# Performance work log

Measured on AMD Instinct MI355X. Metric: run time of the kernel, lower is better.

## Reference

```python
import jax, jax.numpy as jnp
import numpy as np

B, S, D, H = 2, 2048, 2048, 16
HD = D // H  # head_dim = 128


def setup_inputs() -> dict:
    key = jax.random.key(0)
    ks = jax.random.split(key, 7)
    s = 0.02
    return {
        "q": jax.random.normal(ks[0], (B, S, D), jnp.float32),
        "k": jax.random.normal(ks[1], (B, S, D), jnp.float32),
        "v": jax.random.normal(ks[2], (B, S, D), jnp.float32),
        "wq": jax.random.normal(ks[3], (D, D), jnp.float32) * s,
        "wk": jax.random.normal(ks[4], (D, D), jnp.float32) * s,
        "wv": jax.random.normal(ks[5], (D, D), jnp.float32) * s,
        "wo": jax.random.normal(ks[6], (D, D), jnp.float32) * s,
    }


def reference(q, k, v, wq, wk, wv, wo):
    # Linear(bias=False): y = x @ W.T  (torch weight layout [out, in])
    xq = jnp.einsum("bse,me->bsm", q, wq).reshape(B, S, H, HD).transpose(0, 2, 1, 3)
    xk = jnp.einsum("bse,me->bsm", k, wk).reshape(B, S, H, HD).transpose(0, 2, 1, 3)
    xv = jnp.einsum("bse,me->bsm", v, wv).reshape(B, S, H, HD).transpose(0, 2, 1, 3)
    scores = jnp.einsum("bhqd,bhkd->bhqk", xq, xk) / jnp.sqrt(jnp.float32(HD))
    # causal mask: -inf above diagonal
    causal = jnp.tril(jnp.ones((S, S), dtype=bool))
    scores = jnp.where(causal[None, None], scores, jnp.float32(-jnp.inf))
    probs = jax.nn.softmax(scores.astype(jnp.float32), axis=-1)
    out = jnp.einsum("bhqk,bhkd->bhqd", probs, xv)  # [B,H,S,HD]
    out = out.transpose(0, 2, 1, 3).reshape(B, S, D)
    out = jnp.einsum("bsm,em->bse", out, wo)
    return out
```

## Files before the change

### kernel.cpp

```cpp
#include <hip/hip_runtime.h>

typedef __bf16 bf16x8 __attribute__((ext_vector_type(8)));
typedef float f32x4 __attribute__((ext_vector_type(4)));

__device__ inline unsigned short f2bf(float f) {
  unsigned int u = __float_as_uint(f);
  u = (u + 0x7FFFu + ((u >> 16) & 1u)) >> 16;
  return (unsigned short)u;
}

__device__ inline void gl_lds16(const void* g, void* l) {
  __builtin_amdgcn_global_load_lds(
      (__attribute__((address_space(1))) const void*)g,
      (__attribute__((address_space(3))) void*)l, 16, 0, 0);
}

__global__ __launch_bounds__(256) void cvt_batch(const float* __restrict__ p0,
                                                 const float* __restrict__ p1,
                                                 const float* __restrict__ p2,
                                                 const float* __restrict__ p3,
                                                 unsigned short* __restrict__ out,
                                                 int n4each) {
  const int y = blockIdx.y;
  const float* src = (y == 0) ? p0 : (y == 1) ? p1 : (y == 2) ? p2 : p3;
  unsigned short* dst = out + (size_t)y * n4each * 4;
  int i = blockIdx.x * 256 + threadIdx.x;
  if (i >= n4each) return;
  const float4 v = ((const float4*)src)[i];
  ushort4 o;
  o.x = f2bf(v.x); o.y = f2bf(v.y); o.z = f2bf(v.z); o.w = f2bf(v.w);
  ((ushort4*)dst)[i] = o;
}

template <int MODE>
__global__ __launch_bounds__(512, 2) void gemm8(const unsigned short* __restrict__ A,
                                                const unsigned short* __restrict__ Wb,
                                                void* __restrict__ Cv,
                                                int N, int Kloop, int lda,
                                                float qscale) {
  extern __shared__ char lds[];
  const int tid = threadIdx.x;
  const int w = tid >> 6, l = tid & 63;
  const int wr = w >> 2, wc = w & 3;

  const int nbx = N >> 8;
  const int cpx = gridDim.x >> 3;
  const int bid = blockIdx.x;
  const int swz = (bid & 7) * cpx + (bid >> 3);
  const int by = swz / nbx, bx = swz % nbx;
  const int m0 = by << 7, n0 = bx << 8;

  const unsigned short* W = Wb;
  const unsigned short* Ab = A;
  float scale = 1.0f;
  int seg = 0;
  if (MODE == 0) {
    seg = m0 >> 12;
    W = Wb + (size_t)seg * 2048 * 2048;
    scale = (seg == 0) ? qscale : 1.0f;
  }

  const int col_l = ((l & 3) * 8) ^ ((l >= 32) ? 16 : 0);
  const size_t rowA0 = (size_t)(m0 + w * 16 + (l >> 2)) * lda + col_l;
  const size_t rowB0 = (size_t)(n0 + w * 16 + (l >> 2)) * lda + col_l;
  const size_t rowB1 = rowB0 + (size_t)128 * lda;
  const int stA = w * 2048;

  const int Sread = ((l & 15) * 64 + (l >> 4) * 16) ^ ((l & 8) << 2);
  const int ldsAr = Sread;
  const int ldsBr = 16384 + (wc >> 1) * 16384 + Sread;

  const f32x4 fz = {0.f, 0.f, 0.f, 0.f};
  f32x4 acc[4][4];
#pragma unroll
  for (int i = 0; i < 4; i++)
#pragma unroll
    for (int j = 0; j < 4; j++) acc[i][j] = fz;
  bf16x8 afA[2][2], afB[2][2], bfr[2][4];

#define STAGE_A(pb, kb)                               \
  gl_lds16(Ab + rowA0 + (kb), (pb) + stA);            \
  gl_lds16(Ab + rowA0 + (kb) + 32, (pb) + stA + 1024)

#define STAGE_B(pb, h, kb)                                                \
  gl_lds16(W + ((h) ? rowB1 : rowB0) + (kb),                              \
           (pb) + 16384 + (h) * 16384 + stA);                             \
  gl_lds16(W + ((h) ? rowB1 : rowB0) + (kb) + 32,                         \
           (pb) + 16384 + (h) * 16384 + stA + 1024)

#define LDF(dst, pb, qi)                                                       \
  _Pragma("unroll") for (int i = 0; i < 2; ++i) {                              \
    dst[0][i] =                                                                \
        *(const bf16x8*)((pb) + ldsAr + (wr * 4 + (qi) * 2 + i) * 2048);       \
    dst[1][i] = *(const bf16x8*)((pb) + ldsAr +                                \
                                 (wr * 4 + (qi) * 2 + i) * 2048 + 1024);       \
  }

#define LDB(pb, qj)                                                            \
  _Pragma("unroll") for (int j = 0; j < 2; ++j) {                              \
    bfr[0][(qj) * 2 + j] = *(const bf16x8*)(                                   \
        (pb) + ldsBr + ((wc & 1) * 4 + (qj) * 2 + j) * 2048);                  \
    bfr[1][(qj) * 2 + j] = *(const bf16x8*)(                                   \
        (pb) + ldsBr + ((wc & 1) * 4 + (qj) * 2 + j) * 2048 + 1024);           \
  }

#define MM_ALL(AF, qi)                                                         \
  _Pragma("unroll") for (int ks = 0; ks < 2; ++ks)                             \
      _Pragma("unroll") for (int i = 0; i < 2; ++i)                            \
          _Pragma("unroll") for (int j = 0; j < 4; ++j)                        \
              acc[(qi) * 2 + i][j] = __builtin_amdgcn_mfma_f32_16x16x32_bf16(  \
                  AF[ks][i], bfr[ks][j], acc[(qi) * 2 + i][j], 0, 0, 0)

#define BAR                      \
  __builtin_amdgcn_s_barrier(); \
  __builtin_amdgcn_sched_barrier(0)
#define WV6                                         \
  asm volatile("s_waitcnt vmcnt(6)" ::: "memory"); \
  __builtin_amdgcn_sched_barrier(0)
#define PRIO1 __builtin_amdgcn_s_setprio(1)
#define PRIO0 __builtin_amdgcn_s_setprio(0)

  char* p0 = lds;
  char* p1 = lds + 49152;
  char* p2 = lds + 98304;

  STAGE_A(p0, 0);
  STAGE_B(p0, 0, 0);
  STAGE_B(p0, 1, 0);
  STAGE_A(p1, 64);
  STAGE_B(p1, 0, 64);
  STAGE_B(p1, 1, 64);
  WV6;
  BAR;

  const int NT = Kloop >> 6;
  for (int it = 0; it < NT; ++it) {
    int t2 = it + 2;
    if (t2 >= NT) t2 -= NT;
    const int tk2 = t2 * 64;

    LDF(afA, p0, 0);
    LDB(p0, 0);
    LDB(p0, 1);
    LDF(afB, p0, 1);
    STAGE_A(p2, tk2);
    STAGE_B(p2, 0, tk2);
    STAGE_B(p2, 1, tk2);
    __builtin_amdgcn_sched_barrier(0);
    PRIO1;
    MM_ALL(afA, 0);
    MM_ALL(afB, 1);
    PRIO0;
    WV6;
    BAR;
    char* tp = p0; p0 = p1; p1 = p2; p2 = tp;
  }
  asm volatile("s_waitcnt vmcnt(0)" ::: "memory");
  __builtin_amdgcn_sched_barrier(0);

  const int erow = m0 + wr * 64 + (l >> 4) * 4;
  const int ecol = n0 + wc * 64 + (l & 15);
  if (MODE == 0) {
    unsigned short* C = (unsigned short*)Cv;
    if (seg == 2) {
      const int b = (m0 - 8192) >> 11;
      const int s0 = ((m0 - 8192) & 2047) + wr * 64 + ((l >> 4) << 2);
      unsigned short* VT = C + (size_t)2 * 4096 * 2048;
#pragma unroll
      for (int i = 0; i < 4; i++)
#pragma unroll
        for (int j = 0; j < 4; j++) {
          const int c = ecol + j * 16;
          ushort4 o;
          o.x = f2bf(acc[i][j][0]); o.y = f2bf(acc[i][j][1]);
          o.z = f2bf(acc[i][j][2]); o.w = f2bf(acc[i][j][3]);
          *(ushort4*)&VT[((size_t)((b << 4) + (c >> 7)) * 128 + (c & 127)) * 2048 +
                         s0 + i * 16] = o;
        }
    } else {
#pragma unroll
      for (int i = 0; i < 4; i++)
#pragma unroll
        for (int j = 0; j < 4; j++)
#pragma unroll
          for (int r = 0; r < 4; r++)
            C[(size_t)(erow + i * 16 + r) * N + ecol + j * 16] =
                f2bf(acc[i][j][r] * scale);
    }
  } else {
    float* C = (float*)Cv;
#pragma unroll
    for (int i = 0; i < 4; i++)
#pragma unroll
      for (int j = 0; j < 4; j++)
#pragma unroll
        for (int r = 0; r < 4; r++)
          C[(size_t)(erow + i * 16 + r) * N + ecol + j * 16] = acc[i][j][r];
  }
#undef STAGE_A
#undef STAGE_B
#undef LDF
#undef LDB
#undef MM_ALL
#undef BAR
#undef WV6
#undef PRIO1
#undef PRIO0
}

__global__ __launch_bounds__(256) void flash_attn(const unsigned short* __restrict__ Qb,
                                                  const unsigned short* __restrict__ Kb,
                                                  const unsigned short* __restrict__ Vt,
                                                  unsigned short* __restrict__ Ob) {
  extern __shared__ char flds[];
  const int h = blockIdx.x, b = blockIdx.y;
  const int tile = 31 - blockIdx.z;
  const int q0 = tile * 64;
  const int tid = threadIdx.x;
  const int w = tid >> 6, l = tid & 63;
  const int lm = l & 15, lk = l >> 4;

  bf16x8 qf[4];
  {
    const unsigned short* qr = Qb + (size_t)(b * 2048 + q0 + w * 16 + lm) * 2048 + h * 128;
    for (int dc = 0; dc < 4; dc++) qf[dc] = *(const bf16x8*)&qr[dc * 32 + lk * 8];
  }

  const f32x4 fz = {0.f, 0.f, 0.f, 0.f};
  float l_r[4] = {0.f, 0.f, 0.f, 0.f};
  f32x4 oacc[8];
  for (int jd = 0; jd < 8; jd++) oacc[jd] = fz;

  const int nkt = tile + 1;
  unsigned short* Pw = (unsigned short*)(flds + 65536) + w * 1024;

#define FSTAGE(kti, bi)                                                              \
  do {                                                                               \
    const int kt_ = (kti)*64;                                                        \
    unsigned short* kls = (unsigned short*)(flds + (bi)*16384);                      \
    unsigned short* vls = (unsigned short*)(flds + 32768 + (bi)*16384);              \
    for (int iss = 0; iss < 4; iss++)                                                \
      gl_lds16(Kb + (size_t)(b * 2048 + kt_ + w * 16 + lm) * 2048 + h * 128 +        \
                   (iss * 4 + lk) * 8,                                               \
               kls + (w * 16 + iss * 4) * 128);                                      \
    for (int t = 0; t < 2; t++) {                                                    \
      int dg = w * 2 + t;                                                            \
      for (int c = 0; c < 2; c++)                                                    \
        gl_lds16(Vt + (size_t)((b * 16 + h) * 128 + dg * 16 + lm) * 2048 + kt_ +     \
                     (c * 4 + lk) * 8,                                               \
                 vls + (dg * 8 + c * 4) * 128);                                      \
    }                                                                                \
  } while (0)

#define FBAR                     \
  __builtin_amdgcn_s_barrier(); \
  __builtin_amdgcn_sched_barrier(0)

  FSTAGE(0, 0);
  if (nkt > 1) FSTAGE(1, 1);
  asm volatile("s_waitcnt vmcnt(0)" ::: "memory");
  __builtin_amdgcn_sched_barrier(0);
  FBAR;

  for (int kti = 0; kti < nkt; kti++) {
    const int cur = kti & 1;
    const int kt = kti * 64;
    const unsigned short* lsKc = (const unsigned short*)(flds + cur * 16384);
    const unsigned short* lsVc = (const unsigned short*)(flds + 32768 + cur * 16384);

    f32x4 s[4];
    for (int jn = 0; jn < 4; jn++) s[jn] = fz;
    __builtin_amdgcn_s_setprio(1);
    for (int jn = 0; jn < 4; jn++)
      for (int dc = 0; dc < 4; dc++) {
        bf16x8 kf = *(const bf16x8*)&lsKc[(jn * 16 + dc * 4) * 128 + l * 8];
        s[jn] = __builtin_amdgcn_mfma_f32_16x16x32_bf16(qf[dc], kf, s[jn], 0, 0, 0);
      }
    __builtin_amdgcn_s_setprio(0);

    const int diag = (kt == q0);
    for (int jn = 0; jn < 4; jn++) {
      int kcol = kt + jn * 16 + lm;
      for (int r = 0; r < 4; r++) {
        int qrow = q0 + w * 16 + lk * 4 + r;
        float p = (diag && kcol > qrow) ? 0.0f : __expf(s[jn][r]);
        s[jn][r] = p;
        l_r[r] += p;
      }
    }

    for (int jn = 0; jn < 4; jn++)
      for (int r = 0; r < 4; r++)
        Pw[(jn * 2 + (lm >> 3)) * 128 + (lk * 4 + r) * 8 + (lm & 7)] = f2bf(s[jn][r]);

    __builtin_amdgcn_s_setprio(1);
    for (int c = 0; c < 2; c++) {
      bf16x8 pf = *(const bf16x8*)&Pw[c * 512 + l * 8];
      for (int jd = 0; jd < 8; jd++) {
        bf16x8 vf = *(const bf16x8*)&lsVc[(jd * 8 + c * 4) * 128 + l * 8];
        oacc[jd] = __builtin_amdgcn_mfma_f32_16x16x32_bf16(pf, vf, oacc[jd], 0, 0, 0);
      }
    }
    __builtin_amdgcn_s_setprio(0);

    FBAR;
    if (kti + 2 < nkt) {
      FSTAGE(kti + 2, cur);
      asm volatile("s_waitcnt vmcnt(8)" ::: "memory");
    } else {
      asm volatile("s_waitcnt vmcnt(0)" ::: "memory");
    }
    __builtin_amdgcn_sched_barrier(0);
    FBAR;
  }

  for (int r = 0; r < 4; r++)
    for (int off = 1; off < 16; off <<= 1) l_r[r] += __shfl_xor(l_r[r], off, 64);

  for (int jd = 0; jd < 8; jd++) {
    int dcol = h * 128 + jd * 16 + lm;
    for (int r = 0; r < 4; r++) {
      size_t idx = (size_t)(b * 2048 + q0 + w * 16 + lk * 4 + r) * 2048 + dcol;
      Ob[idx] = f2bf(oacc[jd][r] / l_r[r]);
    }
  }
#undef FSTAGE
#undef FBAR
}

extern "C" void kernel_launch(void* const* d_in, const int* in_sizes, int n_in,
                              void* d_out, int out_size, void* d_ws, size_t ws_size,
                              hipStream_t stream) {
  const float* q  = (const float*)d_in[0];
  const float* k  = (const float*)d_in[1];
  const float* v  = (const float*)d_in[2];
  const float* wq = (const float*)d_in[3];
  const float* wk = (const float*)d_in[4];
  const float* wv = (const float*)d_in[5];
  const float* wo = (const float*)d_in[6];
  float* out = (float*)d_out;

  static bool attr_done = false;
  if (!attr_done) {
    hipFuncSetAttribute((const void*)gemm8<0>,
                        hipFuncAttributeMaxDynamicSharedMemorySize, 147456);
    hipFuncSetAttribute((const void*)gemm8<1>,
                        hipFuncAttributeMaxDynamicSharedMemorySize, 147456);
    hipFuncSetAttribute((const void*)flash_attn,
                        hipFuncAttributeMaxDynamicSharedMemorySize, 73728);
    attr_done = true;
  }

  const size_t SD = (size_t)4096 * 2048;
  const size_t DD = (size_t)2048 * 2048;
  unsigned short* ws  = (unsigned short*)d_ws;
  unsigned short* qb  = ws;
  unsigned short* wqb = qb + 3 * SD;
  unsigned short* wob = wqb + 3 * DD;
  unsigned short* Qb  = wqb + 4 * DD;
  unsigned short* Kb  = Qb + SD;
  unsigned short* VT  = Kb + SD;
  unsigned short* Ob  = qb + SD;

  cvt_batch<<<dim3(8192, 3), 256, 0, stream>>>(q, k, v, q, qb, (int)(SD / 4));
  cvt_batch<<<dim3(4096, 4), 256, 0, stream>>>(wq, wk, wv, wo, wqb, (int)(DD / 4));

  gemm8<0><<<dim3(768), 512, 147456, stream>>>(qb, wqb, (void*)Qb, 2048, 2048,
                                               2048, 0.08838834764831845f);

  flash_attn<<<dim3(16, 2, 32), 256, 73728, stream>>>(Qb, Kb, VT, Ob);

  gemm8<1><<<dim3(256), 512, 147456, stream>>>(Ob, wob, (void*)out, 2048, 2048,
                                               2048, 1.0f);
}
```

Measured before the change: 415.4 us.

## Double flash-attn query tile per block, single-buffer V, merge conversion launches

The flash attention kernel now handles 128 query rows per block, with each wave processing two 16-row query slices that share every K and V fragment read from LDS. This halves K/V global traffic and the number of blocks. V is single-buffered and K double-buffered, with loads issued between the two MFMA phases and an extra barrier per iteration. LDS use drops to 64KB so two blocks can fit per CU. The two fp32-to-bf16 conversion launches are merged into one 7-row grid to save a launch. The trade-offs are fewer blocks (512 instead of 1024), a load-imbalanced causal grid, and higher register pressure from the doubled accumulators.

```diff
diff --git a/kernel.cpp b/kernel.cpp
--- a/kernel.cpp
+++ b/kernel.cpp
@@ -15,21 +15,27 @@
       (__attribute__((address_space(3))) void*)l, 16, 0, 0);
 }
 
-__global__ __launch_bounds__(256) void cvt_batch(const float* __restrict__ p0,
-                                                 const float* __restrict__ p1,
-                                                 const float* __restrict__ p2,
-                                                 const float* __restrict__ p3,
-                                                 unsigned short* __restrict__ out,
-                                                 int n4each) {
+__global__ __launch_bounds__(256) void cvt_all(const float* __restrict__ q,
+                                               const float* __restrict__ k,
+                                               const float* __restrict__ v,
+                                               const float* __restrict__ wq,
+                                               const float* __restrict__ wk,
+                                               const float* __restrict__ wv,
+                                               const float* __restrict__ wo,
+                                               unsigned short* __restrict__ out) {
+  const int SD4 = 2097152, DD4 = 1048576;
   const int y = blockIdx.y;
-  const float* src = (y == 0) ? p0 : (y == 1) ? p1 : (y == 2) ? p2 : p3;
-  unsigned short* dst = out + (size_t)y * n4each * 4;
-  int i = blockIdx.x * 256 + threadIdx.x;
-  if (i >= n4each) return;
-  const float4 v = ((const float4*)src)[i];
+  const int n4 = (y < 3) ? SD4 : DD4;
+  const int i = blockIdx.x * 256 + threadIdx.x;
+  if (i >= n4) return;
+  const float* src = (y == 0) ? q : (y == 1) ? k : (y == 2) ? v
+                    : (y == 3) ? wq : (y == 4) ? wk : (y == 5) ? wv : wo;
+  const size_t dst4 = (y < 3) ? (size_t)y * SD4
+                              : (size_t)3 * SD4 + (size_t)(y - 3) * DD4;
+  const float4 f = ((const float4*)src)[i];
   ushort4 o;
-  o.x = f2bf(v.x); o.y = f2bf(v.y); o.z = f2bf(v.z); o.w = f2bf(v.w);
-  ((ushort4*)dst)[i] = o;
+  o.x = f2bf(f.x); o.y = f2bf(f.y); o.z = f2bf(f.z); o.w = f2bf(f.w);
+  ((ushort4*)out)[dst4 + i] = o;
 }
 
 template <int MODE>
@@ -208,124 +214,142 @@
 #undef PRIO0
 }
 
-__global__ __launch_bounds__(256) void flash_attn(const unsigned short* __restrict__ Qb,
-                                                  const unsigned short* __restrict__ Kb,
-                                                  const unsigned short* __restrict__ Vt,
-                                                  unsigned short* __restrict__ Ob) {
+__global__ __launch_bounds__(256, 2) void flash_attn(const unsigned short* __restrict__ Qb,
+                                                     const unsigned short* __restrict__ Kb,
+                                                     const unsigned short* __restrict__ Vt,
+                                                     unsigned short* __restrict__ Ob) {
   extern __shared__ char flds[];
+  unsigned short* const LS = (unsigned short*)flds;
   const int h = blockIdx.x, b = blockIdx.y;
-  const int tile = 31 - blockIdx.z;
-  const int q0 = tile * 64;
+  const int tile = 15 - blockIdx.z;
+  const int q0 = tile * 128;
   const int tid = threadIdx.x;
   const int w = tid >> 6, l = tid & 63;
   const int lm = l & 15, lk = l >> 4;
 
-  bf16x8 qf[4];
-  {
-    const unsigned short* qr = Qb + (size_t)(b * 2048 + q0 + w * 16 + lm) * 2048 + h * 128;
-    for (int dc = 0; dc < 4; dc++) qf[dc] = *(const bf16x8*)&qr[dc * 32 + lk * 8];
+  unsigned short* const K0 = LS;
+  unsigned short* const K1 = LS + 8192;
+  unsigned short* const Vp = LS + 16384;
+  unsigned short* const Pw = LS + 24576 + w * 2048;
+
+  bf16x8 qf[2][4];
+  for (int qh = 0; qh < 2; qh++) {
+    const unsigned short* qr =
+        Qb + (size_t)(b * 2048 + q0 + w * 32 + qh * 16 + lm) * 2048 + h * 128;
+    for (int dc = 0; dc < 4; dc++) qf[qh][dc] = *(const bf16x8*)&qr[dc * 32 + lk * 8];
   }
 
   const f32x4 fz = {0.f, 0.f, 0.f, 0.f};
-  float l_r[4] = {0.f, 0.f, 0.f, 0.f};
-  f32x4 oacc[8];
-  for (int jd = 0; jd < 8; jd++) oacc[jd] = fz;
-
-  const int nkt = tile + 1;
-  unsigned short* Pw = (unsigned short*)(flds + 65536) + w * 1024;
-
-#define FSTAGE(kti, bi)                                                              \
-  do {                                                                               \
-    const int kt_ = (kti)*64;                                                        \
-    unsigned short* kls = (unsigned short*)(flds + (bi)*16384);                      \
-    unsigned short* vls = (unsigned short*)(flds + 32768 + (bi)*16384);              \
-    for (int iss = 0; iss < 4; iss++)                                                \
-      gl_lds16(Kb + (size_t)(b * 2048 + kt_ + w * 16 + lm) * 2048 + h * 128 +        \
-                   (iss * 4 + lk) * 8,                                               \
-               kls + (w * 16 + iss * 4) * 128);                                      \
-    for (int t = 0; t < 2; t++) {                                                    \
-      int dg = w * 2 + t;                                                            \
-      for (int c = 0; c < 2; c++)                                                    \
-        gl_lds16(Vt + (size_t)((b * 16 + h) * 128 + dg * 16 + lm) * 2048 + kt_ +     \
-                     (c * 4 + lk) * 8,                                               \
-                 vls + (dg * 8 + c * 4) * 128);                                      \
-    }                                                                                \
-  } while (0)
-
+  float l_r[2][4];
+  f32x4 oacc[2][8];
+  for (int qh = 0; qh < 2; qh++) {
+    for (int r = 0; r < 4; r++) l_r[qh][r] = 0.f;
+    for (int jd = 0; jd < 8; jd++) oacc[qh][jd] = fz;
+  }
+
+  const int nkt = 2 * tile + 2;
+
+#define STK(kti, kp)                                                            \
+  for (int iss = 0; iss < 4; iss++)                                             \
+    gl_lds16(Kb + (size_t)(b * 2048 + (kti) * 64 + w * 16 + lm) * 2048 +        \
+                 h * 128 + (iss * 4 + lk) * 8,                                  \
+             (kp) + (w * 16 + iss * 4) * 128)
+#define STV(kti)                                                                \
+  for (int t = 0; t < 2; t++) {                                                 \
+    int dg = w * 2 + t;                                                         \
+    for (int c = 0; c < 2; c++)                                                 \
+      gl_lds16(Vt + (size_t)((b * 16 + h) * 128 + dg * 16 + lm) * 2048 +        \
+                   (kti) * 64 + (c * 4 + lk) * 8,                               \
+               Vp + (dg * 8 + c * 4) * 128);                                    \
+  }
 #define FBAR                     \
   __builtin_amdgcn_s_barrier(); \
   __builtin_amdgcn_sched_barrier(0)
-
-  FSTAGE(0, 0);
-  if (nkt > 1) FSTAGE(1, 1);
-  asm volatile("s_waitcnt vmcnt(0)" ::: "memory");
-  __builtin_amdgcn_sched_barrier(0);
+#define WVD0                                        \
+  asm volatile("s_waitcnt vmcnt(0)" ::: "memory"); \
+  __builtin_amdgcn_sched_barrier(0)
+
+  STV(0);
+  STK(0, K0);
+  STK(1, K1);
+  WVD0;
   FBAR;
 
+  unsigned short* Kc = K0;
+  unsigned short* Kn = K1;
+
   for (int kti = 0; kti < nkt; kti++) {
-    const int cur = kti & 1;
     const int kt = kti * 64;
-    const unsigned short* lsKc = (const unsigned short*)(flds + cur * 16384);
-    const unsigned short* lsVc = (const unsigned short*)(flds + 32768 + cur * 16384);
-
-    f32x4 s[4];
-    for (int jn = 0; jn < 4; jn++) s[jn] = fz;
+
+    f32x4 s[2][4];
+    for (int qh = 0; qh < 2; qh++)
+      for (int jn = 0; jn < 4; jn++) s[qh][jn] = fz;
     __builtin_amdgcn_s_setprio(1);
     for (int jn = 0; jn < 4; jn++)
       for (int dc = 0; dc < 4; dc++) {
-        bf16x8 kf = *(const bf16x8*)&lsKc[(jn * 16 + dc * 4) * 128 + l * 8];
-        s[jn] = __builtin_amdgcn_mfma_f32_16x16x32_bf16(qf[dc], kf, s[jn], 0, 0, 0);
+        bf16x8 kf = *(const bf16x8*)&Kc[(jn * 16 + dc * 4) * 128 + l * 8];
+        s[0][jn] = __builtin_amdgcn_mfma_f32_16x16x32_bf16(qf[0][dc], kf, s[0][jn], 0, 0, 0);
+        s[1][jn] = __builtin_amdgcn_mfma_f32_16x16x32_bf16(qf[1][dc], kf, s[1][jn], 0, 0, 0);
       }
     __builtin_amdgcn_s_setprio(0);
 
-    const int diag = (kt == q0);
-    for (int jn = 0; jn < 4; jn++) {
-      int kcol = kt + jn * 16 + lm;
-      for (int r = 0; r < 4; r++) {
-        int qrow = q0 + w * 16 + lk * 4 + r;
-        float p = (diag && kcol > qrow) ? 0.0f : __expf(s[jn][r]);
-        s[jn][r] = p;
-        l_r[r] += p;
+    for (int qh = 0; qh < 2; qh++) {
+      const int r0 = q0 + w * 32 + qh * 16;
+      const bool mz = (kt + 63 > r0);
+      for (int jn = 0; jn < 4; jn++) {
+        const int kcol = kt + jn * 16 + lm;
+        for (int r = 0; r < 4; r++) {
+          const int qrow = r0 + lk * 4 + r;
+          float p = (mz && kcol > qrow) ? 0.0f : __expf(s[qh][jn][r]);
+          s[qh][jn][r] = p;
+          l_r[qh][r] += p;
+        }
       }
+      for (int jn = 0; jn < 4; jn++)
+        for (int r = 0; r < 4; r++)
+          Pw[qh * 1024 + (jn * 2 + (lm >> 3)) * 128 + (lk * 4 + r) * 8 + (lm & 7)] =
+              f2bf(s[qh][jn][r]);
     }
 
-    for (int jn = 0; jn < 4; jn++)
-      for (int r = 0; r < 4; r++)
-        Pw[(jn * 2 + (lm >> 3)) * 128 + (lk * 4 + r) * 8 + (lm & 7)] = f2bf(s[jn][r]);
+    WVD0;
+    FBAR;
+    if (kti + 2 < nkt) STK(kti + 2, Kc);
 
     __builtin_amdgcn_s_setprio(1);
     for (int c = 0; c < 2; c++) {
-      bf16x8 pf = *(const bf16x8*)&Pw[c * 512 + l * 8];
+      bf16x8 pf0 = *(const bf16x8*)&Pw[c * 512 + l * 8];
+      bf16x8 pf1 = *(const bf16x8*)&Pw[1024 + c * 512 + l * 8];
       for (int jd = 0; jd < 8; jd++) {
-        bf16x8 vf = *(const bf16x8*)&lsVc[(jd * 8 + c * 4) * 128 + l * 8];
-        oacc[jd] = __builtin_amdgcn_mfma_f32_16x16x32_bf16(pf, vf, oacc[jd], 0, 0, 0);
+        bf16x8 vf = *(const bf16x8*)&Vp[(jd * 8 + c * 4) * 128 + l * 8];
+        oacc[0][jd] = __builtin_amdgcn_mfma_f32_16x16x32_bf16(pf0, vf, oacc[0][jd], 0, 0, 0);
+        oacc[1][jd] = __builtin_amdgcn_mfma_f32_16x16x32_bf16(pf1, vf, oacc[1][jd], 0, 0, 0);
       }
     }
     __builtin_amdgcn_s_setprio(0);
 
     FBAR;
-    if (kti + 2 < nkt) {
-      FSTAGE(kti + 2, cur);
-      asm volatile("s_waitcnt vmcnt(8)" ::: "memory");
-    } else {
-      asm volatile("s_waitcnt vmcnt(0)" ::: "memory");
+    if (kti + 1 < nkt) STV(kti + 1);
+
+    unsigned short* tp = Kc; Kc = Kn; Kn = tp;
+  }
+
+  for (int qh = 0; qh < 2; qh++) {
+    for (int r = 0; r < 4; r++)
+      for (int off = 1; off < 16; off <<= 1)
+        l_r[qh][r] += __shfl_xor(l_r[qh][r], off, 64);
+    for (int jd = 0; jd < 8; jd++) {
+      const int dcol = h * 128 + jd * 16 + lm;
+      for (int r = 0; r < 4; r++) {
+        size_t idx =
+            (size_t)(b * 2048 + q0 + w * 32 + qh * 16 + lk * 4 + r) * 2048 + dcol;
+        Ob[idx] = f2bf(oacc[qh][jd][r] / l_r[qh][r]);
+      }
     }
-    __builtin_amdgcn_sched_barrier(0);
-    FBAR;
-  }
-
-  for (int r = 0; r < 4; r++)
-    for (int off = 1; off < 16; off <<= 1) l_r[r] += __shfl_xor(l_r[r], off, 64);
-
-  for (int jd = 0; jd < 8; jd++) {
-    int dcol = h * 128 + jd * 16 + lm;
-    for (int r = 0; r < 4; r++) {
-      size_t idx = (size_t)(b * 2048 + q0 + w * 16 + lk * 4 + r) * 2048 + dcol;
-      Ob[idx] = f2bf(oacc[jd][r] / l_r[r]);
-    }
-  }
-#undef FSTAGE
+  }
+#undef STK
+#undef STV
 #undef FBAR
+#undef WVD0
 }
 
 extern "C" void kernel_launch(void* const* d_in, const int* in_sizes, int n_in,
@@ -347,7 +371,7 @@
     hipFuncSetAttribute((const void*)gemm8<1>,
                         hipFuncAttributeMaxDynamicSharedMemorySize, 147456);
     hipFuncSetAttribute((const void*)flash_attn,
-                        hipFuncAttributeMaxDynamicSharedMemorySize, 73728);
+                        hipFuncAttributeMaxDynamicSharedMemorySize, 65536);
     attr_done = true;
   }
 
@@ -362,13 +386,12 @@
   unsigned short* VT  = Kb + SD;
   unsigned short* Ob  = qb + SD;
 
-  cvt_batch<<<dim3(8192, 3), 256, 0, stream>>>(q, k, v, q, qb, (int)(SD / 4));
-  cvt_batch<<<dim3(4096, 4), 256, 0, stream>>>(wq, wk, wv, wo, wqb, (int)(DD / 4));
+  cvt_all<<<dim3(8192, 7), 256, 0, stream>>>(q, k, v, wq, wk, wv, wo, qb);
 
   gemm8<0><<<dim3(768), 512, 147456, stream>>>(qb, wqb, (void*)Qb, 2048, 2048,
                                                2048, 0.08838834764831845f);
 
-  flash_attn<<<dim3(16, 2, 32), 256, 73728, stream>>>(Qb, Kb, VT, Ob);
+  flash_attn<<<dim3(16, 2, 16), 256, 65536, stream>>>(Qb, Kb, VT, Ob);
 
   gemm8<1><<<dim3(256), 512, 147456, stream>>>(Ob, wob, (void*)out, 2048, 2048,
                                                2048, 1.0f);
```

Result: faster. 405.4 us (-2.4%).
